# Performance work log

Hardware: AMD Instinct MI355X
Metric: run time of the kernel (lower is better)

The kernel has to match this reference:

```python
import jax, jax.numpy as jnp
import numpy as np

PAD_IDX = 1
B, L, E, H = 2, 256, 512, 8
D = E // H
SCALE = D ** -0.5


def setup_inputs() -> dict:
    key = jax.random.key(0)
    ks = jax.random.split(key, 10)
    std = 0.02
    return {
        "queries": jax.random.normal(ks[0], (B, L, E), jnp.float32),
        "keys": jax.random.normal(ks[1], (B, L, E), jnp.float32),
        "values": jax.random.normal(ks[2], (B, L, E), jnp.float32),
        "relation": jax.random.normal(ks[3], (B, L, L, E), jnp.float32),
        "adj_mask": jax.random.randint(ks[4], (B, L, L), 0, 2, jnp.int32),
        "Wq": jax.random.normal(ks[5], (E, E), jnp.float32) * std,
        "bq": jnp.zeros((E,), jnp.float32),
        "Wk": jax.random.normal(ks[6], (E, E), jnp.float32) * std,
        "bk": jnp.zeros((E,), jnp.float32),
        "Wv": jax.random.normal(ks[7], (E, E), jnp.float32) * std,
        "bv": jnp.zeros((E,), jnp.float32),
        "Wr": jax.random.normal(ks[8], (2 * E, E), jnp.float32) * std,
        "Wo": jax.random.normal(ks[9], (E, E), jnp.float32) * std,
        "bo": jnp.zeros((E,), jnp.float32),
    }


def reference(queries, keys, values, relation, adj_mask,
              Wq, bq, Wk, bk, Wv, bv, Wr, Wo, bo):
    b, t, _ = queries.shape
    s = keys.shape[1]
    # input projections (torch Linear: y = x @ W.T + b)
    q = ((queries @ Wq.T + bq) * SCALE).reshape(b, t, H, D)
    k = (keys @ Wk.T + bk).reshape(b, s, H, D)
    v = (values @ Wv.T + bv).reshape(b, s, H, D)
    # relation projection -> relation queries/keys, [b, t, s, H, D] then transpose(1,2)
    rel = relation @ Wr.T                              # [b, t, s, 2E]
    rq, rk = jnp.split(rel, 2, axis=-1)
    rq = rq.reshape(b, t, s, H, D).transpose(0, 2, 1, 3, 4)  # [b, s, t, H, D]
    rk = rk.reshape(b, t, s, H, D).transpose(0, 2, 1, 3, 4)
    # broadcasted relation bias (requires t == s, as in the original)
    qe = q[:, :, None] + rq                            # [b, t, s, H, D]
    ke = k[:, None] + rk                               # [b, t, s, H, D]
    attn = jnp.einsum('bijhn,bijhn->bijh', qe, ke)     # [b, t, s, H]
    pad = (adj_mask == PAD_IDX)[..., None]             # [b, t, s, 1]
    attn = jnp.where(pad, -jnp.inf, attn)
    attn_weights = jax.nn.softmax(attn, axis=2)
    out = jnp.einsum('bijh,bjhn->bihn', attn_weights, v).reshape(b, t, E)
    out = out @ Wo.T + bo
    return out, attn_weights
```

## Files before the change

kernel.cpp:

```cpp
#include <hip/hip_runtime.h>

typedef unsigned int uint32;
typedef __attribute__((ext_vector_type(8))) short bf16x8;
typedef __attribute__((ext_vector_type(4))) float f32x4;


__device__ __forceinline__ uint32 bf_rne(uint32 u) {
  return (u + 0x7fffu + ((u >> 16) & 1u)) >> 16;
}

__global__ void cvt_wr_kernel(const float* __restrict__ Wr, unsigned short* __restrict__ WrBf) {
  int idx = blockIdx.x * 256 + threadIdx.x;
  const uint4* src = (const uint4*)Wr;
  uint4 x = src[idx];
  uint2 o;
  o.x = bf_rne(x.x) | (bf_rne(x.y) << 16);
  o.y = bf_rne(x.z) | (bf_rne(x.w) << 16);
  ((uint2*)WrBf)[idx] = o;
}

__global__ __launch_bounds__(256) void proj_kernel(
    const float* __restrict__ X0, const float* __restrict__ W0, const float* __restrict__ b0, float* __restrict__ Y0,
    const float* __restrict__ X1, const float* __restrict__ W1, const float* __restrict__ b1, float* __restrict__ Y1,
    const float* __restrict__ X2, const float* __restrict__ W2, const float* __restrict__ b2, float* __restrict__ Y2,
    float scale0) {
  int z = blockIdx.z;
  const float* X = (z == 0) ? X0 : (z == 1) ? X1 : X2;
  const float* W = (z == 0) ? W0 : (z == 1) ? W1 : W2;
  const float* bias = (z == 0) ? b0 : (z == 1) ? b1 : b2;
  float* Y = (z == 0) ? Y0 : (z == 1) ? Y1 : Y2;
  float scale = (z == 0) ? scale0 : 1.0f;

  __shared__ float Xs[16][68];
  __shared__ float Ws[16][68];

  int tid = threadIdx.x;
  int tx = tid & 15, ty = tid >> 4;
  int m0 = blockIdx.x * 64, n0 = blockIdx.y * 64;

  float acc[4][4] = {};

  for (int k0 = 0; k0 < 512; k0 += 16) {
#pragma unroll
    for (int u = 0; u < 4; ++u) {
      int idx = tid + u * 256;
      int ml = idx >> 4, kl = idx & 15;
      Xs[kl][ml] = X[(size_t)(m0 + ml) * 512 + k0 + kl];
      Ws[kl][ml] = W[(size_t)(n0 + ml) * 512 + k0 + kl];
    }
    __syncthreads();
#pragma unroll
    for (int kk = 0; kk < 16; ++kk) {
      float4 a = *(const float4*)&Xs[kk][ty * 4];
      float4 w = *(const float4*)&Ws[kk][tx * 4];
      float av[4] = {a.x, a.y, a.z, a.w};
      float wv[4] = {w.x, w.y, w.z, w.w};
#pragma unroll
      for (int i = 0; i < 4; ++i)
#pragma unroll
        for (int jj = 0; jj < 4; ++jj)
          acc[i][jj] += av[i] * wv[jj];
    }
    __syncthreads();
  }
#pragma unroll
  for (int i = 0; i < 4; ++i) {
    int m = m0 + ty * 4 + i;
#pragma unroll
    for (int jj = 0; jj < 4; ++jj) {
      int n = n0 + tx * 4 + jj;
      Y[(size_t)m * 512 + n] = (acc[i][jj] + bias[n]) * scale;
    }
  }
}

__global__ __launch_bounds__(256, 3) void rel_score_kernel(
    const float* __restrict__ rel,
    const unsigned short* __restrict__ wrbf,
    const float* __restrict__ qws,
    const float* __restrict__ kws,
    float* __restrict__ attn)
{
  __shared__ unsigned short As[64 * 72];
  __shared__ float scores[4][64];

  const int tid = threadIdx.x;
  const int lane = tid & 63;
  const int wv = tid >> 6;
  const int blk = blockIdx.x;
  const int hp = blk & 3;
  const int mt = blk >> 2;
  const int b = mt >> 10;
  const int j = (mt >> 2) & 255;
  const int i0 = (mt & 3) << 6;
  const int h0 = hp << 1;

  const float* Abase = rel + (size_t)mt * (64 * 512);

  const int t15 = lane & 15;
  const int kq = (lane >> 4) * 8;

  const unsigned short* bptr[4];
#pragma unroll
  for (int fc = 0; fc < 4; ++fc) {
    int g = (wv & 1) * 4 + fc;
    int wr_row = (g & 1) * 512 + (h0 + (wv >> 1)) * 64 + (g >> 1) * 16 + t15;
    bptr[fc] = wrbf + (size_t)wr_row * 512 + kq;
  }

  const int arow0 = tid >> 3;
  const int ak8 = (tid & 7) * 8;

  f32x4 acc[4][4];
#pragma unroll
  for (int a = 0; a < 4; ++a)
#pragma unroll
    for (int c = 0; c < 4; ++c)
      acc[a][c] = (f32x4){0.f, 0.f, 0.f, 0.f};

  for (int k0 = 0; k0 < 512; k0 += 64) {
    bf16x8 bfr[2][4];
#pragma unroll
    for (int kh = 0; kh < 2; ++kh)
#pragma unroll
      for (int fc = 0; fc < 4; ++fc)
        bfr[kh][fc] = *(const bf16x8*)(bptr[fc] + k0 + kh * 32);
#pragma unroll
    for (int u = 0; u < 2; ++u) {
      int row = arow0 + u * 32;
      const uint4* src = (const uint4*)(Abase + (size_t)row * 512 + k0 + ak8);
      uint4 x = src[0];
      uint4 y = src[1];
      uint4 o;
      o.x = (x.y & 0xffff0000u) | (x.x >> 16);
      o.y = (x.w & 0xffff0000u) | (x.z >> 16);
      o.z = (y.y & 0xffff0000u) | (y.x >> 16);
      o.w = (y.w & 0xffff0000u) | (y.z >> 16);
      *(uint4*)&As[row * 72 + ak8] = o;
    }
    __syncthreads();
#pragma unroll
    for (int kh = 0; kh < 2; ++kh) {
      int kk = kh * 32 + kq;
      bf16x8 af[4];
#pragma unroll
      for (int fr = 0; fr < 4; ++fr)
        af[fr] = *(const bf16x8*)&As[(fr * 16 + t15) * 72 + kk];
#pragma unroll
      for (int fr = 0; fr < 4; ++fr)
#pragma unroll
        for (int fc = 0; fc < 4; ++fc)
          acc[fr][fc] = __builtin_amdgcn_mfma_f32_16x16x32_bf16(
              af[fr], bfr[kh][fc], acc[fr][fc], 0, 0, 0);
    }
    __syncthreads();
  }

  const int hthis = h0 + (wv >> 1);
  const int dbase = (wv & 1) * 32;
  const float* qbase = qws + ((size_t)(b * 256 + i0)) * 512 + hthis * 64;
  const float* krow = kws + ((size_t)(b * 256 + j)) * 512 + hthis * 64;
  const int rgrp = lane >> 4;
#pragma unroll
  for (int fr = 0; fr < 4; ++fr) {
#pragma unroll
    for (int r = 0; r < 4; ++r) {
      int m = fr * 16 + rgrp * 4 + r;
      float s = 0.f;
#pragma unroll
      for (int p = 0; p < 2; ++p) {
        int d = dbase + p * 16 + t15;
        float qv = qbase[(size_t)m * 512 + d];
        float kv = krow[d];
        s += (qv + acc[fr][p * 2][r]) * (kv + acc[fr][p * 2 + 1][r]);
      }
      s += __shfl_xor(s, 1);
      s += __shfl_xor(s, 2);
      s += __shfl_xor(s, 4);
      s += __shfl_xor(s, 8);
      if (t15 == 0) scores[wv][m] = s;
    }
  }
  __syncthreads();
  if (tid < 128) {
    int hl = tid >> 6, m = tid & 63;
    float sc = scores[hl * 2][m] + scores[hl * 2 + 1][m];
    attn[(((size_t)(b * 256 + i0 + m)) * 256 + j) * 8 + (h0 + hl)] = sc;
  }
}

__global__ __launch_bounds__(256) void softmax_av_kernel(
    float* __restrict__ attn, const int* __restrict__ adj,
    const float* __restrict__ vws, float* __restrict__ o1) {
  __shared__ float sl[2048];
  __shared__ int msk[256];
  int bi = blockIdx.x;
  int b = bi >> 8;
  float* base = attn + (size_t)bi * 2048;
  const int* abase = adj + (size_t)bi * 256;
  int tid = threadIdx.x;
#pragma unroll
  for (int u = 0; u < 8; ++u) sl[tid + u * 256] = base[tid + u * 256];
  msk[tid] = abase[tid];
  __syncthreads();
  int h = tid >> 5, l5 = tid & 31;
  float mx = -INFINITY;
#pragma unroll
  for (int u = 0; u < 8; ++u) {
    int jj = l5 + u * 32;
    if (msk[jj] != 1) mx = fmaxf(mx, sl[jj * 8 + h]);
  }
#pragma unroll
  for (int off = 16; off >= 1; off >>= 1) mx = fmaxf(mx, __shfl_xor(mx, off));
  float ev[8];
  float sum = 0.f;
#pragma unroll
  for (int u = 0; u < 8; ++u) {
    int jj = l5 + u * 32;
    float e = (msk[jj] != 1) ? __expf(sl[jj * 8 + h] - mx) : 0.f;
    ev[u] = e;
    sum += e;
  }
#pragma unroll
  for (int off = 16; off >= 1; off >>= 1) sum += __shfl_xor(sum, off);
  float inv = (sum > 0.f) ? (1.f / sum) : 0.f;
#pragma unroll
  for (int u = 0; u < 8; ++u) {
    int jj = l5 + u * 32;
    sl[jj * 8 + h] = ev[u] * inv;
  }
  __syncthreads();
#pragma unroll
  for (int u = 0; u < 8; ++u) base[tid + u * 256] = sl[tid + u * 256];
  const float* vbase = vws + (size_t)b * (256 * 512);
  int e0 = tid, e1 = tid + 256;
  int h0 = e0 >> 6, h1 = e1 >> 6;
  float a0 = 0.f, a1 = 0.f;
  for (int jj = 0; jj < 256; ++jj) {
    float w0 = sl[jj * 8 + h0];
    float w1 = sl[jj * 8 + h1];
    const float* vr = vbase + (size_t)jj * 512;
    a0 += w0 * vr[e0];
    a1 += w1 * vr[e1];
  }
  float* orow = o1 + (size_t)bi * 512;
  orow[e0] = a0;
  orow[e1] = a1;
}

extern "C" void kernel_launch(void* const* d_in, const int* in_sizes, int n_in,
                              void* d_out, int out_size, void* d_ws, size_t ws_size,
                              hipStream_t stream) {
  const float* queries = (const float*)d_in[0];
  const float* keys    = (const float*)d_in[1];
  const float* values  = (const float*)d_in[2];
  const float* relation = (const float*)d_in[3];
  const int*   adj     = (const int*)d_in[4];
  const float* Wq = (const float*)d_in[5];
  const float* bq = (const float*)d_in[6];
  const float* Wk = (const float*)d_in[7];
  const float* bk = (const float*)d_in[8];
  const float* Wv = (const float*)d_in[9];
  const float* bv = (const float*)d_in[10];
  const float* Wr = (const float*)d_in[11];
  const float* Wo = (const float*)d_in[12];
  const float* bo = (const float*)d_in[13];

  float* out  = (float*)d_out;
  float* attn = out + 262144;

  float* ws  = (float*)d_ws;
  float* qws = ws;
  float* kws = ws + 262144;
  float* vws = ws + 524288;
  float* o1  = ws + 786432;
  unsigned short* wrbf = (unsigned short*)(ws + 1048576);

  cvt_wr_kernel<<<dim3(512), dim3(256), 0, stream>>>(Wr, wrbf);

  proj_kernel<<<dim3(8, 8, 3), dim3(256), 0, stream>>>(
      queries, Wq, bq, qws,
      keys,    Wk, bk, kws,
      values,  Wv, bv, vws,
      0.125f);

  rel_score_kernel<<<dim3(8192), dim3(256), 0, stream>>>(relation, wrbf, qws, kws, attn);

  softmax_av_kernel<<<dim3(512), dim3(256), 0, stream>>>(attn, adj, vws, o1);

  proj_kernel<<<dim3(8, 8, 1), dim3(256), 0, stream>>>(
      o1, Wo, bo, out,
      nullptr, nullptr, nullptr, nullptr,
      nullptr, nullptr, nullptr, nullptr,
      1.0f);
}
```

Baseline: 730.9 us.

## Double-buffer relation tile in LDS and prefetch next K-slice into registers

The main GEMM loop in the relation score kernel now keeps two shared-memory A buffers and loads the next 64-wide K slice of the fp32 relation tensor into registers while the current slice is multiplied with MFMA. This removes the second barrier per iteration and lets global loads overlap with matrix math in this memory-bound kernel. It doubles the LDS footprint for A and keeps four extra uint4 registers live, which could lower occupancy under the 3-blocks-per-CU launch bound.

Result: faster. 695.6 us (-4.8%).

```diff
diff --git a/kernel.cpp b/kernel.cpp
--- a/kernel.cpp
+++ b/kernel.cpp
@@ -81,7 +81,7 @@
     const float* __restrict__ kws,
     float* __restrict__ attn)
 {
-  __shared__ unsigned short As[64 * 72];
+  __shared__ unsigned short As[2][64 * 72];
   __shared__ float scores[4][64];
 
   const int tid = threadIdx.x;
@@ -110,6 +110,8 @@
 
   const int arow0 = tid >> 3;
   const int ak8 = (tid & 7) * 8;
+  const uint4* aptr0 = (const uint4*)(Abase + (size_t)arow0 * 512 + ak8);
+  const uint4* aptr1 = (const uint4*)(Abase + (size_t)(arow0 + 32) * 512 + ak8);
 
   f32x4 acc[4][4];
 #pragma unroll
@@ -118,25 +120,40 @@
     for (int c = 0; c < 4; ++c)
       acc[a][c] = (f32x4){0.f, 0.f, 0.f, 0.f};
 
-  for (int k0 = 0; k0 < 512; k0 += 64) {
+  uint4 p0 = aptr0[0];
+  uint4 p1 = aptr0[1];
+  uint4 p2 = aptr1[0];
+  uint4 p3 = aptr1[1];
+
+  for (int k = 0; k < 8; ++k) {
+    const int k0 = k * 64;
     bf16x8 bfr[2][4];
 #pragma unroll
     for (int kh = 0; kh < 2; ++kh)
 #pragma unroll
       for (int fc = 0; fc < 4; ++fc)
         bfr[kh][fc] = *(const bf16x8*)(bptr[fc] + k0 + kh * 32);
-#pragma unroll
-    for (int u = 0; u < 2; ++u) {
-      int row = arow0 + u * 32;
-      const uint4* src = (const uint4*)(Abase + (size_t)row * 512 + k0 + ak8);
-      uint4 x = src[0];
-      uint4 y = src[1];
+    unsigned short* asb = As[k & 1];
+    {
       uint4 o;
-      o.x = (x.y & 0xffff0000u) | (x.x >> 16);
-      o.y = (x.w & 0xffff0000u) | (x.z >> 16);
-      o.z = (y.y & 0xffff0000u) | (y.x >> 16);
-      o.w = (y.w & 0xffff0000u) | (y.z >> 16);
-      *(uint4*)&As[row * 72 + ak8] = o;
+      o.x = (p0.y & 0xffff0000u) | (p0.x >> 16);
+      o.y = (p0.w & 0xffff0000u) | (p0.z >> 16);
+      o.z = (p1.y & 0xffff0000u) | (p1.x >> 16);
+      o.w = (p1.w & 0xffff0000u) | (p1.z >> 16);
+      *(uint4*)&asb[arow0 * 72 + ak8] = o;
+      o.x = (p2.y & 0xffff0000u) | (p2.x >> 16);
+      o.y = (p2.w & 0xffff0000u) | (p2.z >> 16);
+      o.z = (p3.y & 0xffff0000u) | (p3.x >> 16);
+      o.w = (p3.w & 0xffff0000u) | (p3.z >> 16);
+      *(uint4*)&asb[(arow0 + 32) * 72 + ak8] = o;
+    }
+    if (k < 7) {
+      const uint4* n0p = (const uint4*)((const float*)aptr0 + (k + 1) * 64);
+      const uint4* n1p = (const uint4*)((const float*)aptr1 + (k + 1) * 64);
+      p0 = n0p[0];
+      p1 = n0p[1];
+      p2 = n1p[0];
+      p3 = n1p[1];
     }
     __syncthreads();
 #pragma unroll
@@ -145,7 +162,7 @@
       bf16x8 af[4];
 #pragma unroll
       for (int fr = 0; fr < 4; ++fr)
-        af[fr] = *(const bf16x8*)&As[(fr * 16 + t15) * 72 + kk];
+        af[fr] = *(const bf16x8*)&asb[(fr * 16 + t15) * 72 + kk];
 #pragma unroll
       for (int fr = 0; fr < 4; ++fr)
 #pragma unroll
@@ -153,7 +170,6 @@
           acc[fr][fc] = __builtin_amdgcn_mfma_f32_16x16x32_bf16(
               af[fr], bfr[kh][fc], acc[fr][fc], 0, 0, 0);
     }
-    __syncthreads();
   }
 
   const int hthis = h0 + (wv >> 1);
```

## Restructure relation-score GEMM into per-wave tiles with register prefetch and no block syncs

Applied to the files above, without the earlier changes.

The relation-score kernel is reorganised so each block handles a single head and each wave owns 32 query rows. Each wave stages its bf16-packed relation slice in a private double-buffered LDS region, so the block-wide __syncthreads are gone. The next K-slice of the fp32 relation is prefetched into registers while the current one is consumed by MFMAs. Each wave now computes the full 64-dim head, so the dot product is reduced within the wave and written straight to attn, dropping the cross-wave LDS score reduction. In exchange, every relation row is loaded once per head instead of once per head pair, relying on L2 to absorb the extra traffic. Wr fragments are also re-read from global memory inside the inner loop.

Measured after the change: 1.119 ms. 1.53x slower.

```diff
diff --git a/kernel.cpp b/kernel.cpp
--- a/kernel.cpp
+++ b/kernel.cpp
@@ -81,111 +81,94 @@
     const float* __restrict__ kws,
     float* __restrict__ attn)
 {
-  __shared__ unsigned short As[64 * 72];
-  __shared__ float scores[4][64];
+  __shared__ unsigned short As[4][2][32 * 72];
 
   const int tid = threadIdx.x;
   const int lane = tid & 63;
   const int wv = tid >> 6;
   const int blk = blockIdx.x;
-  const int hp = blk & 3;
-  const int mt = blk >> 2;
-  const int b = mt >> 10;
-  const int j = (mt >> 2) & 255;
-  const int i0 = (mt & 3) << 6;
-  const int h0 = hp << 1;
-
-  const float* Abase = rel + (size_t)mt * (64 * 512);
+  const int head = blk & 7;
+  const int mt2 = blk >> 3;
+  const int b = mt2 >> 9;
+  const int j = (mt2 >> 1) & 255;
+  const int ih = mt2 & 1;
+  const int i0 = ih * 128 + wv * 32;
+
+  const float* Abase = rel + (((size_t)(b * 256 + j)) * 256 + i0) * 512;
 
   const int t15 = lane & 15;
-  const int kq = (lane >> 4) * 8;
-
-  const unsigned short* bptr[4];
-#pragma unroll
-  for (int fc = 0; fc < 4; ++fc) {
-    int g = (wv & 1) * 4 + fc;
-    int wr_row = (g & 1) * 512 + (h0 + (wv >> 1)) * 64 + (g >> 1) * 16 + t15;
-    bptr[fc] = wrbf + (size_t)wr_row * 512 + kq;
-  }
-
-  const int arow0 = tid >> 3;
-  const int ak8 = (tid & 7) * 8;
-
-  f32x4 acc[4][4];
-#pragma unroll
-  for (int a = 0; a < 4; ++a)
-#pragma unroll
-    for (int c = 0; c < 4; ++c)
-      acc[a][c] = (f32x4){0.f, 0.f, 0.f, 0.f};
-
-  for (int k0 = 0; k0 < 512; k0 += 64) {
-    bf16x8 bfr[2][4];
-#pragma unroll
-    for (int kh = 0; kh < 2; ++kh)
-#pragma unroll
-      for (int fc = 0; fc < 4; ++fc)
-        bfr[kh][fc] = *(const bf16x8*)(bptr[fc] + k0 + kh * 32);
-#pragma unroll
-    for (int u = 0; u < 2; ++u) {
-      int row = arow0 + u * 32;
-      const uint4* src = (const uint4*)(Abase + (size_t)row * 512 + k0 + ak8);
-      uint4 x = src[0];
-      uint4 y = src[1];
-      uint4 o;
-      o.x = (x.y & 0xffff0000u) | (x.x >> 16);
-      o.y = (x.w & 0xffff0000u) | (x.z >> 16);
-      o.z = (y.y & 0xffff0000u) | (y.x >> 16);
-      o.w = (y.w & 0xffff0000u) | (y.z >> 16);
-      *(uint4*)&As[row * 72 + ak8] = o;
-    }
-    __syncthreads();
+  const int q2 = lane >> 4;
+  const int kq = q2 * 8;
+
+  const int arow = q2;
+  const int acol = t15 * 4;
+
+  const unsigned short* bbase = wrbf + ((size_t)(head * 64 + t15)) * 512 + kq;
+
+  f32x4 acc[2][8];
+#pragma unroll
+  for (int fr = 0; fr < 2; ++fr)
+#pragma unroll
+    for (int fc = 0; fc < 8; ++fc)
+      acc[fr][fc] = (f32x4){0.f, 0.f, 0.f, 0.f};
+
+  uint4 a[8];
+#pragma unroll
+  for (int i = 0; i < 8; ++i)
+    a[i] = *(const uint4*)(Abase + (size_t)(4 * i + arow) * 512 + acol);
+
+  for (int k = 0; k < 8; ++k) {
+    const int k0 = k * 64;
+    unsigned short* asb = &As[wv][k & 1][0];
+#pragma unroll
+    for (int i = 0; i < 8; ++i) {
+      uint2 o;
+      o.x = (a[i].y & 0xffff0000u) | (a[i].x >> 16);
+      o.y = (a[i].w & 0xffff0000u) | (a[i].z >> 16);
+      *(uint2*)&asb[(4 * i + arow) * 72 + acol] = o;
+    }
+    if (k < 7) {
+#pragma unroll
+      for (int i = 0; i < 8; ++i)
+        a[i] = *(const uint4*)(Abase + (size_t)(4 * i + arow) * 512 + (k0 + 64) + acol);
+    }
 #pragma unroll
     for (int kh = 0; kh < 2; ++kh) {
-      int kk = kh * 32 + kq;
-      bf16x8 af[4];
-#pragma unroll
-      for (int fr = 0; fr < 4; ++fr)
-        af[fr] = *(const bf16x8*)&As[(fr * 16 + t15) * 72 + kk];
-#pragma unroll
-      for (int fr = 0; fr < 4; ++fr)
-#pragma unroll
-        for (int fc = 0; fc < 4; ++fc)
-          acc[fr][fc] = __builtin_amdgcn_mfma_f32_16x16x32_bf16(
-              af[fr], bfr[kh][fc], acc[fr][fc], 0, 0, 0);
-    }
-    __syncthreads();
-  }
-
-  const int hthis = h0 + (wv >> 1);
-  const int dbase = (wv & 1) * 32;
-  const float* qbase = qws + ((size_t)(b * 256 + i0)) * 512 + hthis * 64;
-  const float* krow = kws + ((size_t)(b * 256 + j)) * 512 + hthis * 64;
-  const int rgrp = lane >> 4;
-#pragma unroll
-  for (int fr = 0; fr < 4; ++fr) {
+      bf16x8 af0 = *(const bf16x8*)&asb[t15 * 72 + kh * 32 + kq];
+      bf16x8 af1 = *(const bf16x8*)&asb[(16 + t15) * 72 + kh * 32 + kq];
+#pragma unroll
+      for (int fc = 0; fc < 8; ++fc) {
+        const int ofs = ((fc & 1) * 512 + (fc >> 1) * 16) * 512;
+        bf16x8 bf = *(const bf16x8*)(bbase + ofs + k0 + kh * 32);
+        acc[0][fc] = __builtin_amdgcn_mfma_f32_16x16x32_bf16(af0, bf, acc[0][fc], 0, 0, 0);
+        acc[1][fc] = __builtin_amdgcn_mfma_f32_16x16x32_bf16(af1, bf, acc[1][fc], 0, 0, 0);
+      }
+    }
+  }
+
+  const float* qbase = qws + ((size_t)(b * 256 + i0)) * 512 + head * 64;
+  const float* krow = kws + ((size_t)(b * 256 + j)) * 512 + head * 64;
+  float kv[4];
+#pragma unroll
+  for (int dc = 0; dc < 4; ++dc) kv[dc] = krow[dc * 16 + t15];
+#pragma unroll
+  for (int fr = 0; fr < 2; ++fr) {
 #pragma unroll
     for (int r = 0; r < 4; ++r) {
-      int m = fr * 16 + rgrp * 4 + r;
+      int m = fr * 16 + q2 * 4 + r;
       float s = 0.f;
 #pragma unroll
-      for (int p = 0; p < 2; ++p) {
-        int d = dbase + p * 16 + t15;
-        float qv = qbase[(size_t)m * 512 + d];
-        float kv = krow[d];
-        s += (qv + acc[fr][p * 2][r]) * (kv + acc[fr][p * 2 + 1][r]);
+      for (int dc = 0; dc < 4; ++dc) {
+        float qv = qbase[(size_t)m * 512 + dc * 16 + t15];
+        s += (qv + acc[fr][dc * 2][r]) * (kv[dc] + acc[fr][dc * 2 + 1][r]);
       }
       s += __shfl_xor(s, 1);
       s += __shfl_xor(s, 2);
       s += __shfl_xor(s, 4);
       s += __shfl_xor(s, 8);
-      if (t15 == 0) scores[wv][m] = s;
-    }
-  }
-  __syncthreads();
-  if (tid < 128) {
-    int hl = tid >> 6, m = tid & 63;
-    float sc = scores[hl * 2][m] + scores[hl * 2 + 1][m];
-    attn[(((size_t)(b * 256 + i0 + m)) * 256 + j) * 8 + (h0 + hl)] = sc;
+      if (t15 == 0)
+        attn[(((size_t)(b * 256 + i0 + m)) * 256 + j) * 8 + head] = s;
+    }
   }
 }
 
```
